# Optimization experiments

Hardware: AMD Instinct MI355X
Metric: run time of the kernel (lower is better)

Reference implementation:

```python
import jax, jax.numpy as jnp
import numpy as np

V, J, NB, NP = 100000, 24, 10, 207
PARENT = np.array([-1, 0, 0, 0, 1, 2, 3, 4, 5, 6, 7, 8, 9, 9, 9, 12, 13, 14, 16, 17, 18, 19, 20, 21])


def setup_inputs() -> dict:
    key = jax.random.key(0)
    ks = jax.random.split(key, 9)
    return {
        "beta": jax.random.normal(ks[0], (NB,), jnp.float32),
        "pose": jax.random.normal(ks[1], (J, 3), jnp.float32),
        "trans": jax.random.normal(ks[2], (3,), jnp.float32),
        "shapedirs": jax.random.normal(ks[3], (V, 3, NB), jnp.float32),
        "v_template": jax.random.normal(ks[4], (V, 3), jnp.float32),
        "J_regressor": jax.random.uniform(ks[5], (J, V), jnp.float32),
        "posedirs": jax.random.normal(ks[6], (V, 3, NP), jnp.float32),
        "weights": jax.random.uniform(ks[7], (V, J), jnp.float32),
        "faces": jax.random.randint(ks[8], (200000, 3), 0, V, jnp.int32),
    }


def _rodrigues(r):
    # r: [N,3] axis-angle -> [N,3,3] rotation matrices
    theta = jnp.sqrt(jnp.sum(r * r, axis=1, keepdims=True)) + 1e-8  # [N,1]
    rh = r / theta
    c = jnp.cos(theta)[:, :, None]  # [N,1,1]
    s = jnp.sin(theta)[:, :, None]
    z = jnp.zeros_like(rh[:, 0])
    K = jnp.stack([z, -rh[:, 2], rh[:, 1],
                   rh[:, 2], z, -rh[:, 0],
                   -rh[:, 1], rh[:, 0], z], axis=1).reshape(-1, 3, 3)
    outer = rh[:, :, None] * rh[:, None, :]
    I = jnp.eye(3, dtype=r.dtype)
    return c * I + (1.0 - c) * outer + s * K


def _with_zeros(Rt):
    # [3,4] -> [4,4] homogeneous
    bottom = jnp.array([[0.0, 0.0, 0.0, 1.0]], dtype=Rt.dtype)
    return jnp.concatenate([Rt, bottom], axis=0)


def reference(beta, pose, trans, shapedirs, v_template, J_regressor, posedirs, weights, faces):
    # shape blending
    v_shaped = jnp.einsum('vdb,b->vd', shapedirs, beta) + v_template  # [V,3]
    Jts = J_regressor @ v_shaped  # [J,3]
    R = _rodrigues(pose)  # [J,3,3]
    # pose blending: lrotmin = (R[1:] - I).flatten(), length 207
    lrotmin = (R[1:] - jnp.eye(3, dtype=R.dtype)).reshape(-1)
    v_posed = v_shaped + jnp.einsum('vdp,p->vd', posedirs, lrotmin)
    # forward kinematics along the 24-joint chain
    G = [_with_zeros(jnp.concatenate([R[0], Jts[0][:, None]], axis=1))]
    for i in range(1, J):
        p = int(PARENT[i])
        loc = _with_zeros(jnp.concatenate([R[i], (Jts[i] - Jts[p])[:, None]], axis=1))
        G.append(G[p] @ loc)
    stacked = jnp.stack(G, axis=0)  # [J,4,4]
    Jh = jnp.concatenate([Jts, jnp.zeros((J, 1), dtype=Jts.dtype)], axis=1)  # [J,4]
    corr = stacked @ Jh[:, :, None]  # [J,4,1]
    A = stacked - jnp.concatenate([jnp.zeros((J, 4, 3), dtype=stacked.dtype), corr], axis=2)
    # LBS skinning
    T = jnp.einsum('vj,jab->vab', weights, A)  # [V,4,4]
    rest = jnp.concatenate([v_posed, jnp.ones((v_posed.shape[0], 1), dtype=v_posed.dtype)], axis=1)  # [V,4]
    v = jnp.einsum('vab,vb->va', T, rest)[:, :3]
    vertices = v + trans[None, :]
    return vertices, faces
```

## Files before the change

kernel.cpp:

```cpp
#include <hip/hip_runtime.h>

#define V_N 100000
#define J_N 24
#define NB_N 10
#define NP_N 207
#define FLAT_P 621
#define FACE_I 600000
#define CHUNKS 50
#define CHUNK_V 2000
#define K1_BLK 1172
#define F_BLK  587

__device__ __constant__ int PARENT_D[24] = {
    -1, 0, 0, 0, 1, 2, 3, 4, 5, 6, 7, 8, 9, 9, 9, 12, 13, 14, 16, 17, 18, 19, 20, 21
};

typedef __attribute__((address_space(3))) void lds_void;
typedef __attribute__((address_space(1))) void glb_void;

__device__ __forceinline__ float wave_sum64(float x) {
    float t;
    t = __int_as_float(__builtin_amdgcn_update_dpp(0, __float_as_int(x), 0x111, 0xf, 0xf, true)); x += t;
    t = __int_as_float(__builtin_amdgcn_update_dpp(0, __float_as_int(x), 0x112, 0xf, 0xf, true)); x += t;
    t = __int_as_float(__builtin_amdgcn_update_dpp(0, __float_as_int(x), 0x114, 0xf, 0xf, true)); x += t;
    t = __int_as_float(__builtin_amdgcn_update_dpp(0, __float_as_int(x), 0x118, 0xf, 0xf, true)); x += t;
    t = __int_as_float(__builtin_amdgcn_update_dpp(0, __float_as_int(x), 0x142, 0xa, 0xf, true)); x += t;
    t = __int_as_float(__builtin_amdgcn_update_dpp(0, __float_as_int(x), 0x143, 0xc, 0xf, true)); x += t;
    return __int_as_float(__builtin_amdgcn_readlane(__float_as_int(x), 63));
}

__global__ __launch_bounds__(256) void kA_shape_faces(const float* __restrict__ shapedirs,
                                                      const float* __restrict__ vtemp,
                                                      const float* __restrict__ beta,
                                                      float* __restrict__ vshaped,
                                                      const int4* __restrict__ faces4,
                                                      float* __restrict__ out) {
    int b = blockIdx.x;
    if (b < K1_BLK) {
        int i = b * 256 + threadIdx.x;
        if (i >= V_N * 3) return;
        const float2* sd2 = reinterpret_cast<const float2*>(shapedirs + (size_t)i * NB_N);
        float2 p0 = sd2[0], p1 = sd2[1], p2 = sd2[2], p3 = sd2[3], p4 = sd2[4];
        float acc = vtemp[i];
        acc += p0.x * beta[0] + p0.y * beta[1];
        acc += p1.x * beta[2] + p1.y * beta[3];
        acc += p2.x * beta[4] + p2.y * beta[5];
        acc += p3.x * beta[6] + p3.y * beta[7];
        acc += p4.x * beta[8] + p4.y * beta[9];
        vshaped[i] = acc;
    } else {
        int i = (b - K1_BLK) * 256 + threadIdx.x;
        if (i < FACE_I / 4) {
            int4 f = faces4[i];
            float4* fdst = reinterpret_cast<float4*>(out + 300000);
            fdst[i] = make_float4((float)f.x, (float)f.y, (float)f.z, (float)f.w);
        }
    }
}

__global__ __launch_bounds__(256) void kB_partial(const float* __restrict__ Jreg,
                                                  const float* __restrict__ vshaped,
                                                  float* __restrict__ partials) {
    int c = blockIdx.x, j = blockIdx.y;
    int t = threadIdx.x;
    const float* row = Jreg + (size_t)j * V_N + (size_t)c * CHUNK_V;
    const float* vs  = vshaped + (size_t)c * CHUNK_V * 3;
    float s0 = 0.f, s1 = 0.f, s2 = 0.f;
    for (int i = t; i < CHUNK_V; i += 256) {
        float w = row[i];
        s0 += w * vs[i * 3 + 0];
        s1 += w * vs[i * 3 + 1];
        s2 += w * vs[i * 3 + 2];
    }
    for (int off = 32; off > 0; off >>= 1) {
        s0 += __shfl_xor(s0, off, 64);
        s1 += __shfl_xor(s1, off, 64);
        s2 += __shfl_xor(s2, off, 64);
    }
    __shared__ float ls[3][4];
    int wv = t >> 6;
    if ((t & 63) == 0) { ls[0][wv] = s0; ls[1][wv] = s1; ls[2][wv] = s2; }
    __syncthreads();
    if (t == 0) {
        float* p = partials + (size_t)c * 72 + j * 3;
        p[0] = ls[0][0] + ls[0][1] + ls[0][2] + ls[0][3];
        p[1] = ls[1][0] + ls[1][1] + ls[1][2] + ls[1][3];
        p[2] = ls[2][0] + ls[2][1] + ls[2][2] + ls[2][3];
    }
}

__global__ __launch_bounds__(128) void kC_fk(const float* __restrict__ pose,
                                             const float* __restrict__ partials,
                                             float* __restrict__ ws_lrot,
                                             float* __restrict__ ws_A) {
    __shared__ float R[24][9];
    __shared__ float G[24][12];
    __shared__ float Jts[24][3];
    int t = threadIdx.x;
    if (t < 72) {
        float s = 0.f;
        #pragma unroll
        for (int c = 0; c < CHUNKS; ++c) s += partials[c * 72 + t];
        (&Jts[0][0])[t] = s;
    }
    if (t < 24) {
        float x = pose[t * 3 + 0], y = pose[t * 3 + 1], z = pose[t * 3 + 2];
        float th = sqrtf(x * x + y * y + z * z) + 1e-8f;
        float inv = 1.0f / th;
        float rx = x * inv, ry = y * inv, rz = z * inv;
        float c = cosf(th), s = sinf(th), ic = 1.0f - c;
        R[t][0] = c + ic * rx * rx;      R[t][1] = ic * rx * ry - s * rz;  R[t][2] = ic * rx * rz + s * ry;
        R[t][3] = ic * ry * rx + s * rz; R[t][4] = c + ic * ry * ry;       R[t][5] = ic * ry * rz - s * rx;
        R[t][6] = ic * rz * rx - s * ry; R[t][7] = ic * rz * ry + s * rx;  R[t][8] = c + ic * rz * rz;
    }
    __syncthreads();
    for (int f = t; f < 640; f += 128) {
        float val = 0.0f;
        if (f < FLAT_P) {
            int p = f % NP_N;
            int j = 1 + p / 9;
            int e = p % 9;
            val = R[j][e] - ((e == 0 || e == 4 || e == 8) ? 1.0f : 0.0f);
        }
        ws_lrot[f] = val;
    }
    if (t < 12) {
        int r = t >> 2, c = t & 3;
        G[0][t] = (c < 3) ? R[0][r * 3 + c] : Jts[0][r];
    }
    __syncthreads();
    for (int i = 1; i < J_N; ++i) {
        int p = PARENT_D[i];
        if (t < 12) {
            int r = t >> 2, c = t & 3;
            float sum = (c == 3) ? G[p][r * 4 + 3] : 0.0f;
            #pragma unroll
            for (int k = 0; k < 3; ++k) {
                float loc = (c < 3) ? R[i][k * 3 + c] : (Jts[i][k] - Jts[p][k]);
                sum += G[p][r * 4 + k] * loc;
            }
            G[i][t] = sum;
        }
        __syncthreads();
    }
    if (t < 72) {
        int j = t / 3, r = t % 3;
        float g0 = G[j][r * 4 + 0], g1 = G[j][r * 4 + 1], g2 = G[j][r * 4 + 2], g3 = G[j][r * 4 + 3];
        float corr = g0 * Jts[j][0] + g1 * Jts[j][1] + g2 * Jts[j][2];
        ws_A[j * 12 + r * 4 + 0] = g0;
        ws_A[j * 12 + r * 4 + 1] = g1;
        ws_A[j * 12 + r * 4 + 2] = g2;
        ws_A[j * 12 + r * 4 + 3] = g3 - corr;
    }
}

__global__ __launch_bounds__(256) void kD_main(const float* __restrict__ posedirs,
                                               const float* __restrict__ weights,
                                               const float* __restrict__ vshaped,
                                               const float* __restrict__ ws_lrot,
                                               const float* __restrict__ ws_A,
                                               const float* __restrict__ trans,
                                               float* __restrict__ out) {
    __shared__ __align__(16) float sP[4 * FLAT_P];
    __shared__ float sL[640];
    __shared__ float sA[288];
    int tid = threadIdx.x;
    int lane = tid & 63;
    int w = tid >> 6;

    const char* gbase = reinterpret_cast<const char*>(posedirs) + (size_t)blockIdx.x * 9936;
    char* lbase = reinterpret_cast<char*>(sP);
    #pragma unroll
    for (int k = 0; k < 3; ++k) {
        int chunk = w + k * 4;
        if (chunk < 10) {
            int nbytes_lanes = (chunk == 9) ? 45 : 64;
            if (lane < nbytes_lanes) {
                const void* g = gbase + chunk * 1024 + lane * 16;
                __builtin_amdgcn_global_load_lds((const glb_void*)g,
                                                 (lds_void*)(lbase + chunk * 1024),
                                                 16, 0, 0);
            }
        }
    }
    for (int i = tid; i < 640; i += 256) sL[i] = ws_lrot[i];
    for (int i = tid; i < 288; i += 256) sA[i] = ws_A[i];
    __syncthreads();

    int v = blockIdx.x * 4 + w;

    const float* pd = sP + w * FLAT_P;
    float a0 = 0.f, a1 = 0.f, a2 = 0.f;
    #pragma unroll
    for (int k = 0; k < 10; ++k) {
        int f = lane + k * 64;
        if (f < FLAT_P) {
            float val = pd[f] * sL[f];
            if (f < 207)      a0 += val;
            else if (f < 414) a1 += val;
            else              a2 += val;
        }
    }
    float vp0 = wave_sum64(a0) + vshaped[v * 3 + 0];
    float vp1 = wave_sum64(a1) + vshaped[v * 3 + 1];
    float vp2 = wave_sum64(a2) + vshaped[v * 3 + 2];

    float r0 = 0.f, r1 = 0.f, r2 = 0.f;
    if (lane < J_N) {
        float wgt = weights[(size_t)v * J_N + lane];
        const float* A = &sA[lane * 12];
        r0 = wgt * (A[0] * vp0 + A[1] * vp1 + A[2]  * vp2 + A[3]);
        r1 = wgt * (A[4] * vp0 + A[5] * vp1 + A[6]  * vp2 + A[7]);
        r2 = wgt * (A[8] * vp0 + A[9] * vp1 + A[10] * vp2 + A[11]);
    }
    float s0 = wave_sum64(r0);
    float s1 = wave_sum64(r1);
    float s2 = wave_sum64(r2);

    if (lane < 3) {
        float res = (lane == 0) ? s0 : (lane == 1) ? s1 : s2;
        out[v * 3 + lane] = res + trans[lane];
    }
}

extern "C" void kernel_launch(void* const* d_in, const int* in_sizes, int n_in,
                              void* d_out, int out_size, void* d_ws, size_t ws_size,
                              hipStream_t stream) {
    const float* beta      = (const float*)d_in[0];
    const float* pose      = (const float*)d_in[1];
    const float* trans     = (const float*)d_in[2];
    const float* shapedirs = (const float*)d_in[3];
    const float* v_template= (const float*)d_in[4];
    const float* J_reg     = (const float*)d_in[5];
    const float* posedirs  = (const float*)d_in[6];
    const float* weights   = (const float*)d_in[7];
    const int*   faces     = (const int*)d_in[8];

    float* out = (float*)d_out;

    float* ws       = (float*)d_ws;
    float* vshaped  = ws;
    float* ws_lrot  = ws + 300080;
    float* ws_A     = ws + 300720;
    float* partials = ws + 301008;

    kA_shape_faces<<<K1_BLK + F_BLK, 256, 0, stream>>>(shapedirs, v_template, beta, vshaped,
                                                       (const int4*)faces, out);
    kB_partial<<<dim3(CHUNKS, J_N), 256, 0, stream>>>(J_reg, vshaped, partials);
    kC_fk<<<1, 128, 0, stream>>>(pose, partials, ws_lrot, ws_A);
    kD_main<<<V_N / 4, 256, 0, stream>>>(posedirs, weights, vshaped, ws_lrot, ws_A, trans, out);
}
```

Baseline: 81.17 us.

## Double-buffer posedirs LDS DMA across multiple vertex groups per block

The main skinning kernel now has each block process ten 4-vertex groups instead of one. It prefetches the next group's posedirs slice into a second LDS buffer through global_load_lds while the current group is being computed. This is meant to overlap memory transfer with compute and to amortise the per-block loading of the lrot and A tables. In exchange, the grid is ten times smaller and LDS use per block doubles, so fewer loads may be in flight across the GPU and the last wave of blocks may be poorly balanced.

```diff
diff --git a/kernel.cpp b/kernel.cpp
--- a/kernel.cpp
+++ b/kernel.cpp
@@ -10,6 +10,8 @@
 #define CHUNK_V 2000
 #define K1_BLK 1172
 #define F_BLK  587
+#define GPB 10
+#define GRP_B 9936
 
 __device__ __constant__ int PARENT_D[24] = {
     -1, 0, 0, 0, 1, 2, 3, 4, 5, 6, 7, 8, 9, 9, 9, 12, 13, 14, 16, 17, 18, 19, 20, 21
@@ -161,65 +163,76 @@
                                                const float* __restrict__ ws_A,
                                                const float* __restrict__ trans,
                                                float* __restrict__ out) {
-    __shared__ __align__(16) float sP[4 * FLAT_P];
+    __shared__ __align__(16) float sP[2][4 * FLAT_P];
     __shared__ float sL[640];
     __shared__ float sA[288];
     int tid = threadIdx.x;
     int lane = tid & 63;
     int w = tid >> 6;
 
-    const char* gbase = reinterpret_cast<const char*>(posedirs) + (size_t)blockIdx.x * 9936;
-    char* lbase = reinterpret_cast<char*>(sP);
-    #pragma unroll
-    for (int k = 0; k < 3; ++k) {
-        int chunk = w + k * 4;
-        if (chunk < 10) {
-            int nbytes_lanes = (chunk == 9) ? 45 : 64;
-            if (lane < nbytes_lanes) {
-                const void* g = gbase + chunk * 1024 + lane * 16;
-                __builtin_amdgcn_global_load_lds((const glb_void*)g,
-                                                 (lds_void*)(lbase + chunk * 1024),
-                                                 16, 0, 0);
+    auto do_dma = [&](int group, int buf) {
+        const char* gb = reinterpret_cast<const char*>(posedirs) + (size_t)group * GRP_B;
+        char* lb = reinterpret_cast<char*>(sP[buf]);
+        #pragma unroll
+        for (int k = 0; k < 3; ++k) {
+            int chunk = w + k * 4;
+            if (chunk < 10) {
+                int nlanes = (chunk == 9) ? 45 : 64;
+                if (lane < nlanes) {
+                    __builtin_amdgcn_global_load_lds(
+                        (const glb_void*)(gb + chunk * 1024 + lane * 16),
+                        (lds_void*)(lb + chunk * 1024), 16, 0, 0);
+                }
             }
         }
-    }
+    };
+
+    int g0 = blockIdx.x * GPB;
+    do_dma(g0, 0);
     for (int i = tid; i < 640; i += 256) sL[i] = ws_lrot[i];
     for (int i = tid; i < 288; i += 256) sA[i] = ws_A[i];
     __syncthreads();
 
-    int v = blockIdx.x * 4 + w;
-
-    const float* pd = sP + w * FLAT_P;
-    float a0 = 0.f, a1 = 0.f, a2 = 0.f;
-    #pragma unroll
-    for (int k = 0; k < 10; ++k) {
-        int f = lane + k * 64;
-        if (f < FLAT_P) {
-            float val = pd[f] * sL[f];
-            if (f < 207)      a0 += val;
-            else if (f < 414) a1 += val;
-            else              a2 += val;
-        }
-    }
-    float vp0 = wave_sum64(a0) + vshaped[v * 3 + 0];
-    float vp1 = wave_sum64(a1) + vshaped[v * 3 + 1];
-    float vp2 = wave_sum64(a2) + vshaped[v * 3 + 2];
-
-    float r0 = 0.f, r1 = 0.f, r2 = 0.f;
-    if (lane < J_N) {
-        float wgt = weights[(size_t)v * J_N + lane];
-        const float* A = &sA[lane * 12];
-        r0 = wgt * (A[0] * vp0 + A[1] * vp1 + A[2]  * vp2 + A[3]);
-        r1 = wgt * (A[4] * vp0 + A[5] * vp1 + A[6]  * vp2 + A[7]);
-        r2 = wgt * (A[8] * vp0 + A[9] * vp1 + A[10] * vp2 + A[11]);
-    }
-    float s0 = wave_sum64(r0);
-    float s1 = wave_sum64(r1);
-    float s2 = wave_sum64(r2);
-
-    if (lane < 3) {
-        float res = (lane == 0) ? s0 : (lane == 1) ? s1 : s2;
-        out[v * 3 + lane] = res + trans[lane];
+    int cur = 0;
+    #pragma unroll 1
+    for (int g = 0; g < GPB; ++g) {
+        if (g + 1 < GPB) do_dma(g0 + g + 1, cur ^ 1);
+
+        int v = (g0 + g) * 4 + w;
+        const float* pd = sP[cur] + w * FLAT_P;
+        float a0 = 0.f, a1 = 0.f, a2 = 0.f;
+        #pragma unroll
+        for (int k = 0; k < 10; ++k) {
+            int f = lane + k * 64;
+            if (f < FLAT_P) {
+                float val = pd[f] * sL[f];
+                if (f < 207)      a0 += val;
+                else if (f < 414) a1 += val;
+                else              a2 += val;
+            }
+        }
+        float vp0 = wave_sum64(a0) + vshaped[v * 3 + 0];
+        float vp1 = wave_sum64(a1) + vshaped[v * 3 + 1];
+        float vp2 = wave_sum64(a2) + vshaped[v * 3 + 2];
+
+        float r0 = 0.f, r1 = 0.f, r2 = 0.f;
+        if (lane < J_N) {
+            float wgt = weights[(size_t)v * J_N + lane];
+            const float* A = &sA[lane * 12];
+            r0 = wgt * (A[0] * vp0 + A[1] * vp1 + A[2]  * vp2 + A[3]);
+            r1 = wgt * (A[4] * vp0 + A[5] * vp1 + A[6]  * vp2 + A[7]);
+            r2 = wgt * (A[8] * vp0 + A[9] * vp1 + A[10] * vp2 + A[11]);
+        }
+        float s0 = wave_sum64(r0);
+        float s1 = wave_sum64(r1);
+        float s2 = wave_sum64(r2);
+
+        if (lane < 3) {
+            float res = (lane == 0) ? s0 : (lane == 1) ? s1 : s2;
+            out[v * 3 + lane] = res + trans[lane];
+        }
+        __syncthreads();
+        cur ^= 1;
     }
 }
 
@@ -248,5 +261,5 @@
                                                        (const int4*)faces, out);
     kB_partial<<<dim3(CHUNKS, J_N), 256, 0, stream>>>(J_reg, vshaped, partials);
     kC_fk<<<1, 128, 0, stream>>>(pose, partials, ws_lrot, ws_A);
-    kD_main<<<V_N / 4, 256, 0, stream>>>(posedirs, weights, vshaped, ws_lrot, ws_A, trans, out);
-}
+    kD_main<<<(V_N / 4) / GPB, 256, 0, stream>>>(posedirs, weights, vshaped, ws_lrot, ws_A, trans, out);
+}
```

Result: no change. 80.52 us (-0.8%).

## Process 8 vertices per wave with register double-buffered posedirs loads

Applied to the files above, without the earlier changes.

The main skinning kernel now gives each wave 8 consecutive vertices instead of one, and launches 8x fewer blocks. The per-block LDS staging of posedirs through global_load_lds is dropped; each wave reads posedirs rows straight into registers and prefetches the next vertex's row while reducing the current one. This amortises the per-block setup (loading lrot and A into shared memory, the barrier) over more vertices and overlaps memory latency with compute. In exchange there are far fewer waves to hide latency (3125 blocks), the per-vertex loop is serial, and register use goes up.

```diff
diff --git a/kernel.cpp b/kernel.cpp
--- a/kernel.cpp
+++ b/kernel.cpp
@@ -10,13 +10,11 @@
 #define CHUNK_V 2000
 #define K1_BLK 1172
 #define F_BLK  587
+#define VPW 8
 
 __device__ __constant__ int PARENT_D[24] = {
     -1, 0, 0, 0, 1, 2, 3, 4, 5, 6, 7, 8, 9, 9, 9, 12, 13, 14, 16, 17, 18, 19, 20, 21
 };
-
-typedef __attribute__((address_space(3))) void lds_void;
-typedef __attribute__((address_space(1))) void glb_void;
 
 __device__ __forceinline__ float wave_sum64(float x) {
     float t;
@@ -161,65 +159,78 @@
                                                const float* __restrict__ ws_A,
                                                const float* __restrict__ trans,
                                                float* __restrict__ out) {
-    __shared__ __align__(16) float sP[4 * FLAT_P];
     __shared__ float sL[640];
     __shared__ float sA[288];
     int tid = threadIdx.x;
+    for (int i = tid; i < 640; i += 256) sL[i] = ws_lrot[i];
+    for (int i = tid; i < 288; i += 256) sA[i] = ws_A[i];
+    __syncthreads();
+
     int lane = tid & 63;
     int w = tid >> 6;
-
-    const char* gbase = reinterpret_cast<const char*>(posedirs) + (size_t)blockIdx.x * 9936;
-    char* lbase = reinterpret_cast<char*>(sP);
-    #pragma unroll
-    for (int k = 0; k < 3; ++k) {
-        int chunk = w + k * 4;
-        if (chunk < 10) {
-            int nbytes_lanes = (chunk == 9) ? 45 : 64;
-            if (lane < nbytes_lanes) {
-                const void* g = gbase + chunk * 1024 + lane * 16;
-                __builtin_amdgcn_global_load_lds((const glb_void*)g,
-                                                 (lds_void*)(lbase + chunk * 1024),
-                                                 16, 0, 0);
+    int vbase = (blockIdx.x * 4 + w) * VPW;
+
+    float cf[10];
+    {
+        const float* pd = posedirs + (size_t)vbase * FLAT_P;
+        #pragma unroll
+        for (int k = 0; k < 10; ++k) {
+            int f = lane + k * 64;
+            cf[k] = (f < FLAT_P) ? pd[f] : 0.0f;
+        }
+    }
+
+    #pragma unroll 1
+    for (int i = 0; i < VPW; ++i) {
+        int v = vbase + i;
+
+        float nf[10];
+        if (i + 1 < VPW) {
+            const float* pd = posedirs + (size_t)(v + 1) * FLAT_P;
+            #pragma unroll
+            for (int k = 0; k < 10; ++k) {
+                int f = lane + k * 64;
+                nf[k] = (f < FLAT_P) ? pd[f] : 0.0f;
             }
-        }
-    }
-    for (int i = tid; i < 640; i += 256) sL[i] = ws_lrot[i];
-    for (int i = tid; i < 288; i += 256) sA[i] = ws_A[i];
-    __syncthreads();
-
-    int v = blockIdx.x * 4 + w;
-
-    const float* pd = sP + w * FLAT_P;
-    float a0 = 0.f, a1 = 0.f, a2 = 0.f;
-    #pragma unroll
-    for (int k = 0; k < 10; ++k) {
-        int f = lane + k * 64;
-        if (f < FLAT_P) {
-            float val = pd[f] * sL[f];
-            if (f < 207)      a0 += val;
-            else if (f < 414) a1 += val;
-            else              a2 += val;
-        }
-    }
-    float vp0 = wave_sum64(a0) + vshaped[v * 3 + 0];
-    float vp1 = wave_sum64(a1) + vshaped[v * 3 + 1];
-    float vp2 = wave_sum64(a2) + vshaped[v * 3 + 2];
-
-    float r0 = 0.f, r1 = 0.f, r2 = 0.f;
-    if (lane < J_N) {
-        float wgt = weights[(size_t)v * J_N + lane];
-        const float* A = &sA[lane * 12];
-        r0 = wgt * (A[0] * vp0 + A[1] * vp1 + A[2]  * vp2 + A[3]);
-        r1 = wgt * (A[4] * vp0 + A[5] * vp1 + A[6]  * vp2 + A[7]);
-        r2 = wgt * (A[8] * vp0 + A[9] * vp1 + A[10] * vp2 + A[11]);
-    }
-    float s0 = wave_sum64(r0);
-    float s1 = wave_sum64(r1);
-    float s2 = wave_sum64(r2);
-
-    if (lane < 3) {
-        float res = (lane == 0) ? s0 : (lane == 1) ? s1 : s2;
-        out[v * 3 + lane] = res + trans[lane];
+        } else {
+            #pragma unroll
+            for (int k = 0; k < 10; ++k) nf[k] = 0.0f;
+        }
+
+        float a0 = 0.f, a1 = 0.f, a2 = 0.f;
+        #pragma unroll
+        for (int k = 0; k < 10; ++k) {
+            int f = lane + k * 64;
+            if (f < FLAT_P) {
+                float val = cf[k] * sL[f];
+                if (f < 207)      a0 += val;
+                else if (f < 414) a1 += val;
+                else              a2 += val;
+            }
+        }
+        float vp0 = wave_sum64(a0) + vshaped[v * 3 + 0];
+        float vp1 = wave_sum64(a1) + vshaped[v * 3 + 1];
+        float vp2 = wave_sum64(a2) + vshaped[v * 3 + 2];
+
+        float r0 = 0.f, r1 = 0.f, r2 = 0.f;
+        if (lane < J_N) {
+            float wgt = weights[(size_t)v * J_N + lane];
+            const float* A = &sA[lane * 12];
+            r0 = wgt * (A[0] * vp0 + A[1] * vp1 + A[2]  * vp2 + A[3]);
+            r1 = wgt * (A[4] * vp0 + A[5] * vp1 + A[6]  * vp2 + A[7]);
+            r2 = wgt * (A[8] * vp0 + A[9] * vp1 + A[10] * vp2 + A[11]);
+        }
+        float s0 = wave_sum64(r0);
+        float s1 = wave_sum64(r1);
+        float s2 = wave_sum64(r2);
+
+        if (lane < 3) {
+            float res = (lane == 0) ? s0 : (lane == 1) ? s1 : s2;
+            out[v * 3 + lane] = res + trans[lane];
+        }
+
+        #pragma unroll
+        for (int k = 0; k < 10; ++k) cf[k] = nf[k];
     }
 }
 
@@ -248,5 +259,5 @@
                                                        (const int4*)faces, out);
     kB_partial<<<dim3(CHUNKS, J_N), 256, 0, stream>>>(J_reg, vshaped, partials);
     kC_fk<<<1, 128, 0, stream>>>(pose, partials, ws_lrot, ws_A);
-    kD_main<<<V_N / 4, 256, 0, stream>>>(posedirs, weights, vshaped, ws_lrot, ws_A, trans, out);
-}
+    kD_main<<<V_N / (4 * VPW), 256, 0, stream>>>(posedirs, weights, vshaped, ws_lrot, ws_A, trans, out);
+}
```

After: 74.99 us (median of 2 runs). 1.08x faster.
